# Kernel tuning notes

Measured on AMD Instinct MI355X. Metric: run time of the kernel, lower is better.

## Reference

```python
import jax, jax.numpy as jnp
import numpy as np

I_CH, O_CH = 64, 64
N_NODES, N_EDGES = 20000, 120000


def build_indices(edge_index):
    """Host-side (numpy) replication of the data-dependent index pipeline:
    sort-by-src -> triplets via searchsorted/repeat_interleave -> sort-by-src ->
    prune low-degree half of nodes -> group-by-src (for scatter-mean) -> reindex.
    All shapes depend only on the (constant) int edge_index.
    """
    ei = np.asarray(edge_index)
    ei = ei[:, np.argsort(ei[0], kind='stable')]
    src, tgt = ei[0], ei[1]
    order = np.argsort(tgt, kind='stable')
    stg = tgt[order]
    lb = np.searchsorted(stg, src, side='left')
    ub = np.searchsorted(stg, src, side='right')
    counts = ub - lb
    T = int(counts.sum())
    rep = np.repeat(np.arange(src.shape[0]), counts)
    start = np.cumsum(counts) - counts
    off = np.arange(T) - start[rep]
    hit = order[lb[rep] + off]
    # triplet rows: (SRC[ALL], TGT[ALL], TGT[R])
    tri = np.stack([src[hit], tgt[hit], tgt[rep]])  # [3, T]
    tri = tri[:, np.argsort(tri[0], kind='stable')]
    # remove(): drop edges touching the lowest-degree half of nodes
    deg = np.bincount(tri.ravel())
    low = np.argsort(deg, kind='stable')[: deg.shape[0] // 2]
    keep = np.ones(deg.shape[0], dtype=bool)
    keep[low] = False
    mask = keep[tri[0]] & keep[tri[1]] & keep[tri[2]]
    pos = np.nonzero(mask)[0]
    tri_kept = tri[:, pos]
    # sum(): group kept triplet-edges by source node
    uniq, inv = np.unique(tri_kept[0], return_inverse=True)
    cnt = np.bincount(inv).astype(np.float32)
    # reindex edge_index to compact node ids
    _, new = np.unique(tri_kept, return_inverse=True)
    new_ei = new.reshape(tri_kept.shape).astype(np.int32)
    return tri.astype(np.int32), pos.astype(np.int32), inv.astype(np.int32), int(uniq.shape[0]), cnt, new_ei


def setup_inputs() -> dict:
    key = jax.random.key(0)
    k1, k2, k3, k4 = jax.random.split(key, 4)
    x = jax.random.normal(k1, (N_NODES, I_CH), dtype=jnp.float32)
    edge_index = jax.random.randint(k2, (2, N_EDGES), 0, N_NODES, dtype=jnp.int32)
    # Conv2d(I, O, (3,1)) parameters
    W = 0.05 * jax.random.normal(k3, (O_CH, I_CH, 3, 1), dtype=jnp.float32)
    b = 0.05 * jax.random.normal(k4, (O_CH,), dtype=jnp.float32)
    return {"x": x, "edge_index": edge_index, "W": W, "b": b}


def reference(x, edge_index, W, b):
    tri, pos, inv, U, cnt, new_ei = build_indices(edge_index)
    tri_j = jnp.asarray(tri)
    # gather: INPUT[i,k,t] = x[tri[k,t], i]  -> g is [3, T, I]
    g = x[tri_j]
    # Conv2d(I,O,(3,1)) on [I,3,T] -> [O,1,T]; squeeze the H dim:
    C = jnp.einsum('oik,kti->ot', W[..., 0], g) + b[:, None]  # [O, T]
    Ck = C[:, jnp.asarray(pos)]  # prune edges touching low-degree nodes
    # scatter-mean over destination group (source node of triplet)
    S = jax.ops.segment_sum(Ck.T, jnp.asarray(inv), num_segments=U)  # [U, O]
    x_new = S / jnp.asarray(cnt)[:, None]
    return x_new, jnp.asarray(new_ei)
```

## Files before the change

kernel.cpp:

```cpp
#include <hip/hip_runtime.h>
#include <stdint.h>

typedef uint32_t u32;
typedef unsigned long long u64;

#define LB_TILE 2048

#define S_MAXT 1
#define S_DSTAR 2
#define S_NEED 3
#define S_U 5

__global__ void scan_lb(const u32* __restrict__ in, u32* __restrict__ out, int n,
                        u64* __restrict__ desc){
  __shared__ u32 sh[256];
  __shared__ u32 shPrefix;
  int tid=threadIdx.x, t=blockIdx.x;
  int base = t*LB_TILE + tid*8;
  u32 v[8]; u32 s=0;
#pragma unroll
  for(int k=0;k<8;k++){ u32 xv=(base+k<n)?in[base+k]:0u; v[k]=s; s+=xv; }
  sh[tid]=s; __syncthreads();
  for(int o=1;o<256;o<<=1){
    u32 y=(tid>=o)?sh[tid-o]:0u;
    __syncthreads();
    sh[tid]+=y;
    __syncthreads();
  }
  u32 tileEx = (tid==0)?0u:sh[tid-1];
  u32 agg = sh[255];
  if(tid==0){
    u32 prefix=0u;
    if(t==0){
      atomicExch(&desc[0], ((u64)agg<<32)|2ull);
    } else {
      atomicExch(&desc[t], ((u64)agg<<32)|1ull);
      int j=t-1;
      while(true){
        u64 d=atomicAdd(&desc[j],0ull);
        u32 st=(u32)d;
        if(st==0u) continue;
        prefix += (u32)(d>>32);
        if(st==2u) break;
        --j;
      }
      atomicExch(&desc[t], ((u64)(prefix+agg)<<32)|2ull);
    }
    shPrefix=prefix;
  }
  __syncthreads();
  u32 p=shPrefix+tileEx;
#pragma unroll
  for(int k=0;k<8;k++){ if(base+k<n) out[base+k]=p+v[k]; }
}

__global__ void rx_hist64(const u64* __restrict__ keys, u32* __restrict__ hist,
                          int B, int shift, int chunk, int hostN,
                          const u32* __restrict__ dCount, int cap){
  __shared__ u32 h[256];
  int n = (hostN>=0) ? hostN : (int)(*dCount<(u32)cap?*dCount:(u32)cap);
  h[threadIdx.x]=0u; __syncthreads();
  int base = blockIdx.x*chunk;
  for(int k=threadIdx.x;k<chunk;k+=256){
    int p = base+k;
    if(p<n){ u32 d=(u32)(keys[p]>>shift)&255u; atomicAdd(&h[d],1u); }
  }
  __syncthreads();
  hist[threadIdx.x*B + blockIdx.x] = h[threadIdx.x];
}

__global__ void rx_scatter64(const u64* __restrict__ keys, u64* __restrict__ okeys,
                             const u32* __restrict__ basep, int B, int shift, int chunk,
                             int hostN, const u32* __restrict__ dCount, int cap){
  __shared__ u32 cnt[256];
  int n = (hostN>=0) ? hostN : (int)(*dCount<(u32)cap?*dCount:(u32)cap);
  int lane = threadIdx.x;
  for(int i=lane;i<256;i+=64) cnt[i]=0u;
  __syncthreads();
  int start = blockIdx.x*chunk;
  int rounds = chunk>>6;
  for(int it=0; it<rounds; ++it){
    int p = start + it*64 + lane;
    bool act = (p<n);
    u64 key = act ? keys[p] : 0ull;
    u32 dig = (u32)(key>>shift)&255u;
    u64 m = __ballot(act ? 1 : 0);
    for(int bb=0;bb<8;bb++){
      u64 bl = __ballot((int)((dig>>bb)&1u));
      m &= ((dig>>bb)&1u) ? bl : ~bl;
    }
    u64 lt = (1ull<<lane) - 1ull;
    u32 rb = (u32)__popcll(m & lt);
    u32 c = cnt[dig];
    if(act && rb==0u) atomicAdd(&cnt[dig], (u32)__popcll(m));
    __syncthreads();
    if(act) okeys[basep[dig*B + blockIdx.x] + c + rb] = key;
  }
}

__global__ void k_hist2(const u32* __restrict__ src, const u32* __restrict__ tgt,
                        u32* cntS, u32* cntT, int E){
  int j=blockIdx.x*256+threadIdx.x;
  if(j<E){ atomicAdd(&cntS[src[j]],1u); atomicAdd(&cntT[tgt[j]],1u); }
}

__global__ void k_deg2(const u32* __restrict__ src, const u32* __restrict__ tgt,
                       const u32* __restrict__ cntS, const u32* __restrict__ cntT,
                       u32* deg, int E){
  int e=blockIdx.x*256+threadIdx.x;
  if(e>=E) return;
  u32 s=src[e], t=tgt[e];
  u32 w0=cntS[t]; if(w0) atomicAdd(&deg[s], w0);
  u32 w2=cntT[s]; if(w2) atomicAdd(&deg[t], w2);
}

__global__ void k_degNode(const u32* __restrict__ cntS, const u32* __restrict__ cntT,
                          u32* deg, int NN, int* scal){
  int v=blockIdx.x*256+threadIdx.x;
  if(v>=NN) return;
  u32 d = deg[v] + cntS[v]*cntT[v];
  deg[v]=d;
  if(d) atomicMax(&scal[S_MAXT], v);
}

__global__ void k_degHist(const u32* __restrict__ deg, u32* dh, int NN, const int* __restrict__ scal){
  int v=blockIdx.x*256+threadIdx.x;
  if(v>=NN || v>scal[S_MAXT]) return;
  u32 d=deg[v]; if(d>65535u)d=65535u;
  atomicAdd(&dh[d],1u);
}

__global__ void k_find_dstar(const u32* __restrict__ dh, const u32* __restrict__ dhs, int* scal){
  int d=blockIdx.x*256+threadIdx.x;
  if(d>=65536) return;
  long long kk=(((long long)scal[S_MAXT])+1)>>1;
  if(kk==0){ if(d==0){ scal[S_DSTAR]=-1; scal[S_NEED]=0; } return; }
  long long cum=(long long)dhs[d], h=(long long)dh[d];
  if(cum<=kk-1 && kk-1<cum+h){ scal[S_DSTAR]=d; scal[S_NEED]=(int)(kk-cum); }
}

__global__ void k_ef(const u32* __restrict__ deg, u32* ef, int NN, const int* __restrict__ scal){
  int v=blockIdx.x*256+threadIdx.x;
  if(v>NN) return;
  ef[v] = (v<NN && v<=scal[S_MAXT] && (int)deg[v]==scal[S_DSTAR]) ? 1u:0u;
}

__global__ void k_keep(const u32* __restrict__ deg, const u32* __restrict__ rankEq,
                       u32* keep, int NN, const int* __restrict__ scal){
  int v=blockIdx.x*256+threadIdx.x;
  if(v>=NN) return;
  int d=(int)deg[v]; int ds=scal[S_DSTAR]; int need=scal[S_NEED];
  u32 kp=1u;
  if(d<ds) kp=0u;
  else if(d==ds && (int)rankEq[v]<need) kp=0u;
  keep[v]=kp;
}

__global__ void k_keptCnt(const u32* __restrict__ src, const u32* __restrict__ tgt,
                          const u32* __restrict__ keep, u32* kc, int E){
  int j=blockIdx.x*256+threadIdx.x;
  if(j<E && keep[src[j]]) atomicAdd(&kc[tgt[j]],1u);
}

__global__ void k_mk_ek(const u32* __restrict__ src, const u32* __restrict__ tgt,
                        u64* ek, int E){
  int j=blockIdx.x*256+threadIdx.x;
  if(j<E) ek[j]=((u64)src[j]<<20)|(u64)tgt[j];
}

__global__ void k_mk_a2(const u64* __restrict__ eks, u64* a2, int E){
  int j=blockIdx.x*256+threadIdx.x;
  if(j<E) a2[j]=((eks[j]&0xFFFFFull)<<20)|(u64)j;
}

__global__ void k_cntk(const u64* __restrict__ eks, const u32* __restrict__ keep,
                       const u32* __restrict__ keptCnt, u32* cntk, int E){
  int e=blockIdx.x*256+threadIdx.x;
  if(e>E) return;
  if(e==E){ cntk[e]=0u; return; }
  u64 ke=eks[e];
  u32 s=(u32)(ke>>20), te=(u32)(ke&0xFFFFFull);
  cntk[e] = (keep[s]&keep[te]) ? keptCnt[s] : 0u;
}

__global__ void k_gen_trik(const u64* __restrict__ eks, const u64* __restrict__ a2s,
                           const u32* __restrict__ rp_tgt, const u32* __restrict__ keep,
                           const u32* __restrict__ startk, u64* __restrict__ trig,
                           int E, int cap){
  int e=blockIdx.x*256+threadIdx.x;
  if(e>=E) return;
  u32 c0=startk[e], c1=startk[e+1];
  if(c0>=c1) return;
  u64 ke=eks[e];
  u32 s=(u32)(ke>>20), te=(u32)(ke&0xFFFFFull);
  u32 lb=rp_tgt[s], ub=rp_tgt[s+1];
  u32 idx=c0;
  for(u32 i=lb; i<ub && idx<c1; ++i){
    u32 h=(u32)(a2s[i]&0xFFFFFull);
    u32 hs=(u32)(eks[h]>>20);
    if(keep[hs]){
      if(idx<(u32)cap) trig[idx]=((u64)hs<<30)|((u64)s<<15)|(u64)te;
      ++idx;
    }
  }
}

__global__ void k_heads_present(const u64* __restrict__ tri, u32* hf, u32* present,
                                const u32* __restrict__ dCount, int cap){
  int Tk=(int)(*dCount<(u32)cap?*dCount:(u32)cap);
  int q=blockIdx.x*256+threadIdx.x;
  if(q>cap) return;
  u32 f=0u;
  if(q<Tk){
    u64 key=tri[q];
    f = (q==0 || (key>>30)!=(tri[q-1]>>30)) ? 1u:0u;
    present[key>>30]=1u; present[(key>>15)&0x7FFFu]=1u; present[key&0x7FFFu]=1u;
  }
  hf[q]=f;
}

__global__ void k_gs2(const u32* __restrict__ hf, const u32* __restrict__ hs,
                      u32* gs, int* scal, const u32* __restrict__ dCount, int cap){
  int Tk=(int)(*dCount<(u32)cap?*dCount:(u32)cap);
  int q=blockIdx.x*256+threadIdx.x;
  if(q==0){ int U=(int)hs[Tk]; scal[S_U]=U; gs[U]=(u32)Tk; }
  if(q>=Tk) return;
  if(hf[q]) gs[hs[q+1]-1u]=(u32)q;
}

__global__ void k_write_ei(const u64* __restrict__ tri, const u32* __restrict__ newid,
                           float* out, const int* __restrict__ scal,
                           const u32* __restrict__ dCount, int cap, int out_size){
  int Tk=(int)(*dCount<(u32)cap?*dCount:(u32)cap);
  int q=blockIdx.x*256+threadIdx.x;
  if(q>=Tk) return;
  u64 key=tri[q];
  int bs=scal[S_U]*64;
  int i0=bs+q, i1=bs+Tk+q, i2=bs+2*Tk+q;
  if(i0<out_size) out[i0]=(float)newid[key>>30];
  if(i1<out_size) out[i1]=(float)newid[(key>>15)&0x7FFFu];
  if(i2<out_size) out[i2]=(float)newid[key&0x7FFFu];
}

__global__ __launch_bounds__(256) void k_xnew3(const float* __restrict__ x,
    const float* __restrict__ W, const float* __restrict__ b,
    const u64* __restrict__ tri, const u32* __restrict__ gs,
    float* __restrict__ out, const int* __restrict__ scal){
  __shared__ float Wl[192*65];
  __shared__ float sv[4][192];
  int tid=threadIdx.x;
  for(int j=tid;j<12288;j+=256){
    int r=j%192, o=j/192;
    Wl[r*65+o]=W[j];
  }
  __syncthreads();
  int U=scal[S_U];
  int w=tid>>6, lane=tid&63;
  float bv=b[lane];
  for(int g=blockIdx.x*4+w; g<U; g+=gridDim.x*4){
    u32 q0=gs[g], q1=gs[g+1];
    float a1=0.f,a2=0.f;
    for(u32 q=q0;q<q1;q++){
      u64 key=tri[q];
      a1 += x[(size_t)((key>>15)&0x7FFFull)*64+lane];
      a2 += x[(size_t)(key&0x7FFFull)*64+lane];
    }
    float xu = x[(size_t)(tri[q0]>>30)*64+lane];
    sv[w][lane]=xu; sv[w][64+lane]=a1; sv[w][128+lane]=a2;
    float acc0=0.f, acc12=0.f;
#pragma unroll 4
    for(int ii=0;ii<64;ii++){
      acc0  += Wl[(ii*3+0)*65+lane]*sv[w][ii];
      acc12 += Wl[(ii*3+1)*65+lane]*sv[w][64+ii]
             + Wl[(ii*3+2)*65+lane]*sv[w][128+ii];
    }
    out[(size_t)g*64+lane] = bv + acc0 + acc12/(float)(q1-q0);
  }
}

extern "C" void kernel_launch(void* const* d_in, const int* in_sizes, int n_in,
                              void* d_out, int out_size, void* d_ws, size_t ws_size,
                              hipStream_t stream){
  const float* x = (const float*)d_in[0];
  const int*   ei = (const int*)d_in[1];
  const float* W = (const float*)d_in[2];
  const float* b = (const float*)d_in[3];
  int NN = in_sizes[0]/64;
  int E  = in_sizes[1]/2;
  const u32* src=(const u32*)ei;
  const u32* tgt=(const u32*)(ei+E);

  int KCAP = ((out_size/3 + 1023)/1024)*1024; if(KCAP<1024) KCAP=1024;

  char* base=(char*)d_ws; size_t off=0;
  auto alloc=[&](size_t nInts)->u32*{
    u32* p=(u32*)(base+off);
    off += ( (nInts*4 + 255) & ~(size_t)255 );
    return p;
  };
  int* scal=(int*)alloc(64);
  u32* cntT=alloc(NN+1); u32* cntS=alloc(NN);
  u32* deg=alloc(NN); u32* degHist=alloc(65536);
  u32* present=alloc(NN+1); u32* keptCnt=alloc(NN);
  u64* desc=(u64*)alloc(8192);
  size_t zoneBytes = off;
  u64* ekA=(u64*)alloc(2*(size_t)E); u64* ekB=(u64*)alloc(2*(size_t)E);
  u64* a2A=(u64*)alloc(2*(size_t)E);
  u64* triA=(u64*)alloc(2*(size_t)KCAP); u64* triB=(u64*)alloc(2*(size_t)KCAP);
  u32* rp_tgt=alloc(NN+1);
  u32* cntk=alloc(E+1); u32* startk=alloc(E+1);
  u32* degHistScan=alloc(65536);
  u32* ef=alloc(NN+1); u32* rankEq=alloc(NN+1); u32* keep=alloc(NN);
  u32* newid=alloc(NN+1); u32* gs=alloc(NN+2);
  u32* hf=alloc(KCAP+1); u32* hs=alloc(KCAP+1);
  u32* rxhist=alloc(65536);
  if(off > ws_size) return;
  u64* a2B=ekB;

  size_t descUsed=0;
  auto scan_ex=[&](const u32* in, u32* out, int n){
    int nb=(n+LB_TILE-1)/LB_TILE;
    scan_lb<<<nb,256,0,stream>>>(in,out,n,desc+descUsed);
    descUsed += (size_t)nb;
  };
  auto rx_pass2=[&](const u64* kin, u64* kout, int B, int shift, int chunk,
                    int hostN, const u32* dCount, int cap){
    rx_hist64<<<B,256,0,stream>>>(kin,rxhist,B,shift,chunk,hostN,dCount,cap);
    scan_ex(rxhist,rxhist,256*B);
    rx_scatter64<<<B,64,0,stream>>>(kin,kout,rxhist,B,shift,chunk,hostN,dCount,cap);
  };

  int gE=(E+255)/256, gE1=(E+256)/256;
  int gNN=(NN+255)/256, gNN1=(NN+256)/256;
  int gKC=(KCAP+255)/256, gKC1=(KCAP+256)/256;
  int BE=(E+511)/512;
  int B3=KCAP/1024;

  hipMemsetAsync(base,0,zoneBytes,stream);

  k_hist2<<<gE,256,0,stream>>>(src,tgt,cntS,cntT,E);
  k_deg2<<<gE,256,0,stream>>>(src,tgt,cntS,cntT,deg,E);
  k_degNode<<<gNN,256,0,stream>>>(cntS,cntT,deg,NN,scal);
  k_degHist<<<gNN,256,0,stream>>>(deg,degHist,NN,scal);
  scan_ex(degHist,degHistScan,65536);
  k_find_dstar<<<256,256,0,stream>>>(degHist,degHistScan,scal);
  k_ef<<<gNN1,256,0,stream>>>(deg,ef,NN,scal);
  scan_ex(ef,rankEq,NN+1);
  k_keep<<<gNN,256,0,stream>>>(deg,rankEq,keep,NN,scal);
  k_keptCnt<<<gE,256,0,stream>>>(src,tgt,keep,keptCnt,E);

  scan_ex(cntT,rp_tgt,NN+1);

  k_mk_ek<<<gE,256,0,stream>>>(src,tgt,ekA,E);
  rx_pass2(ekA,ekB,BE,20,512,E,nullptr,0);
  rx_pass2(ekB,ekA,BE,28,512,E,nullptr,0);

  k_mk_a2<<<gE,256,0,stream>>>(ekA,a2A,E);
  rx_pass2(a2A,a2B,BE,20,512,E,nullptr,0);
  rx_pass2(a2B,a2A,BE,28,512,E,nullptr,0);

  k_cntk<<<gE1,256,0,stream>>>(ekA,keep,keptCnt,cntk,E);
  scan_ex(cntk,startk,E+1);

  k_gen_trik<<<gE,256,0,stream>>>(ekA,a2A,rp_tgt,keep,startk,triA,E,KCAP);

  rx_pass2(triA,triB,B3,30,1024,-1,startk+E,KCAP);
  rx_pass2(triB,triA,B3,38,1024,-1,startk+E,KCAP);

  k_heads_present<<<gKC1,256,0,stream>>>(triA,hf,present,startk+E,KCAP);
  scan_ex(hf,hs,KCAP+1);
  scan_ex(present,newid,NN+1);
  k_gs2<<<gKC,256,0,stream>>>(hf,hs,gs,scal,startk+E,KCAP);

  float* outF=(float*)d_out;
  k_write_ei<<<gKC,256,0,stream>>>(triA,newid,outF,scal,startk+E,KCAP,out_size);
  k_xnew3<<<768,256,0,stream>>>(x,W,b,triA,gs,outF,scal);
}
```

Before: 375.5 us.

## Replace radix sorts with onesweep passes and split gather-sum from matmul

Replaces the hist/scan/scatter radix sort triple with a single-kernel onesweep pass that uses decoupled lookback per digit, with the global digit histograms precomputed. Two separate edge sorts are merged into one 4-pass sort over a combined (tgt,src,idx) key. Several small degree and dstar kernels are fused, and the newid and head scans are combined into one scan. The per-group neighbour sum is moved into a load-balanced atomic kernel ahead of the matvec. The aim is fewer launches and better balance across groups, at the cost of extra float atomics, a large zeroed workspace, and spin-wait lookback.

```diff
diff --git a/kernel.cpp b/kernel.cpp
--- a/kernel.cpp
+++ b/kernel.cpp
@@ -5,6 +5,8 @@
 typedef unsigned long long u64;
 
 #define LB_TILE 2048
+#define OW_TILE 1024
+#define RUN 32
 
 #define S_MAXT 1
 #define S_DSTAR 2
@@ -54,89 +56,182 @@
   for(int k=0;k<8;k++){ if(base+k<n) out[base+k]=p+v[k]; }
 }
 
-__global__ void rx_hist64(const u64* __restrict__ keys, u32* __restrict__ hist,
-                          int B, int shift, int chunk, int hostN,
-                          const u32* __restrict__ dCount, int cap){
-  __shared__ u32 h[256];
-  int n = (hostN>=0) ? hostN : (int)(*dCount<(u32)cap?*dCount:(u32)cap);
-  h[threadIdx.x]=0u; __syncthreads();
-  int base = blockIdx.x*chunk;
-  for(int k=threadIdx.x;k<chunk;k+=256){
-    int p = base+k;
-    if(p<n){ u32 d=(u32)(keys[p]>>shift)&255u; atomicAdd(&h[d],1u); }
-  }
-  __syncthreads();
-  hist[threadIdx.x*B + blockIdx.x] = h[threadIdx.x];
-}
-
-__global__ void rx_scatter64(const u64* __restrict__ keys, u64* __restrict__ okeys,
-                             const u32* __restrict__ basep, int B, int shift, int chunk,
-                             int hostN, const u32* __restrict__ dCount, int cap){
-  __shared__ u32 cnt[256];
-  int n = (hostN>=0) ? hostN : (int)(*dCount<(u32)cap?*dCount:(u32)cap);
-  int lane = threadIdx.x;
-  for(int i=lane;i<256;i+=64) cnt[i]=0u;
-  __syncthreads();
-  int start = blockIdx.x*chunk;
-  int rounds = chunk>>6;
-  for(int it=0; it<rounds; ++it){
-    int p = start + it*64 + lane;
-    bool act = (p<n);
-    u64 key = act ? keys[p] : 0ull;
-    u32 dig = (u32)(key>>shift)&255u;
-    u64 m = __ballot(act ? 1 : 0);
+__global__ __launch_bounds__(256) void ow_pass(const u64* __restrict__ in,
+    u64* __restrict__ outk, const u32* __restrict__ gbase, u64* __restrict__ desc,
+    int shift, int hostN, const u32* __restrict__ dCount, int cap){
+  __shared__ u32 hist[256], bd[256], cnt2[256];
+  __shared__ u32 cnt4[4][256];
+  int n = (hostN>=0)?hostN:(int)((*dCount)<(u32)cap?(*dCount):(u32)cap);
+  int tid=threadIdx.x, b=blockIdx.x, w=tid>>6, lane=tid&63;
+  int base=b*OW_TILE;
+  hist[tid]=0u; cnt2[tid]=0u;
+  cnt4[0][tid]=0u; cnt4[1][tid]=0u; cnt4[2][tid]=0u; cnt4[3][tid]=0u;
+  __syncthreads();
+  u64 k[4]; bool act[4];
+#pragma unroll
+  for(int i=0;i<4;i++){
+    int p=base+i*256+tid; act[i]=(p<n);
+    k[i]=act[i]?in[p]:0ull;
+    if(act[i]) atomicAdd(&hist[(u32)(k[i]>>shift)&255u],1u);
+  }
+  __syncthreads();
+  u32 agg=hist[tid];
+  if(b==0){
+    atomicExch(&desc[tid], ((u64)agg<<32)|2ull);
+    bd[tid]=gbase[tid];
+  } else {
+    atomicExch(&desc[(size_t)b*256+tid], ((u64)agg<<32)|1ull);
+    u32 pre=0u; int j=b-1;
+    while(true){
+      u64 d=atomicAdd(&desc[(size_t)j*256+tid],0ull);
+      u32 st=(u32)d;
+      if(st==0u) continue;
+      pre+=(u32)(d>>32);
+      if(st==2u) break;
+      --j;
+    }
+    atomicExch(&desc[(size_t)b*256+tid], ((u64)(pre+agg)<<32)|2ull);
+    bd[tid]=gbase[tid]+pre;
+  }
+  __syncthreads();
+#pragma unroll
+  for(int i=0;i<4;i++){
+    u32 dig=(u32)(k[i]>>shift)&255u;
+    u64 m=__ballot(act[i]?1:0);
     for(int bb=0;bb<8;bb++){
-      u64 bl = __ballot((int)((dig>>bb)&1u));
-      m &= ((dig>>bb)&1u) ? bl : ~bl;
-    }
-    u64 lt = (1ull<<lane) - 1ull;
-    u32 rb = (u32)__popcll(m & lt);
-    u32 c = cnt[dig];
-    if(act && rb==0u) atomicAdd(&cnt[dig], (u32)__popcll(m));
-    __syncthreads();
-    if(act) okeys[basep[dig*B + blockIdx.x] + c + rb] = key;
-  }
-}
-
-__global__ void k_hist2(const u32* __restrict__ src, const u32* __restrict__ tgt,
-                        u32* cntS, u32* cntT, int E){
+      u64 bl=__ballot((int)((dig>>bb)&1u));
+      m &= ((dig>>bb)&1u)?bl:~bl;
+    }
+    u32 rb=(u32)__popcll(m&((1ull<<lane)-1ull));
+    if(act[i]&&rb==0u) cnt4[w][dig]=(u32)__popcll(m);
+    __syncthreads();
+    if(act[i]){
+      u32 off=cnt2[dig]+rb;
+      for(int w2=0;w2<w;w2++) off+=cnt4[w2][dig];
+      outk[bd[dig]+off]=k[i];
+    }
+    __syncthreads();
+    cnt2[tid]+=cnt4[0][tid]+cnt4[1][tid]+cnt4[2][tid]+cnt4[3][tid];
+    cnt4[0][tid]=0u; cnt4[1][tid]=0u; cnt4[2][tid]=0u; cnt4[3][tid]=0u;
+    __syncthreads();
+  }
+}
+
+__global__ void k_prehistE(const u64* __restrict__ keys, u32* __restrict__ hg, int n){
+  __shared__ u32 h[4][256];
+  int tid=threadIdx.x;
+  for(int i=0;i<4;i++) h[i][tid]=0u;
+  __syncthreads();
+#pragma unroll
+  for(int i=0;i<4;i++){
+    int p=blockIdx.x*OW_TILE+i*256+tid;
+    if(p<n){
+      u64 key=keys[p];
+      atomicAdd(&h[0][(u32)(key>>24)&255u],1u);
+      atomicAdd(&h[1][(u32)(key>>32)&255u],1u);
+      atomicAdd(&h[2][(u32)(key>>40)&255u],1u);
+      atomicAdd(&h[3][(u32)(key>>48)&255u],1u);
+    }
+  }
+  __syncthreads();
+  for(int i=0;i<4;i++) if(h[i][tid]) atomicAdd(&hg[i*256+tid],h[i][tid]);
+}
+
+__global__ void k_prehistT(const u64* __restrict__ keys, u32* __restrict__ hg,
+                           const u32* __restrict__ dCount, int cap){
+  __shared__ u32 h[2][256];
+  int n=(int)((*dCount)<(u32)cap?(*dCount):(u32)cap);
+  int tid=threadIdx.x;
+  h[0][tid]=0u; h[1][tid]=0u;
+  __syncthreads();
+#pragma unroll
+  for(int i=0;i<4;i++){
+    int p=blockIdx.x*OW_TILE+i*256+tid;
+    if(p<n){
+      u64 key=keys[p];
+      atomicAdd(&h[0][(u32)(key>>30)&255u],1u);
+      atomicAdd(&h[1][(u32)(key>>38)&255u],1u);
+    }
+  }
+  __syncthreads();
+  if(h[0][tid]) atomicAdd(&hg[tid],h[0][tid]);
+  if(h[1][tid]) atomicAdd(&hg[256+tid],h[1][tid]);
+}
+
+__global__ void k_scan256(const u32* __restrict__ hg, u32* __restrict__ gb, int H){
+  __shared__ u32 sh[256];
+  int t=threadIdx.x;
+  for(int hh=0;hh<H;hh++){
+    u32 v=hg[hh*256+t];
+    sh[t]=v; __syncthreads();
+    for(int o=1;o<256;o<<=1){
+      u32 y=(t>=o)?sh[t-o]:0u; __syncthreads();
+      sh[t]+=y; __syncthreads();
+    }
+    gb[hh*256+t]=sh[t]-v;
+    __syncthreads();
+  }
+}
+
+__global__ void k_edge0(const u32* __restrict__ src, const u32* __restrict__ tgt,
+                        u32* cntS, u32* cntT, u64* keyA, int E){
   int j=blockIdx.x*256+threadIdx.x;
-  if(j<E){ atomicAdd(&cntS[src[j]],1u); atomicAdd(&cntT[tgt[j]],1u); }
-}
-
-__global__ void k_deg2(const u32* __restrict__ src, const u32* __restrict__ tgt,
-                       const u32* __restrict__ cntS, const u32* __restrict__ cntT,
-                       u32* deg, int E){
+  if(j>=E) return;
+  u32 s=src[j], t=tgt[j];
+  atomicAdd(&cntS[s],1u); atomicAdd(&cntT[t],1u);
+  keyA[j]=((u64)t<<40)|((u64)s<<24)|(u64)j;
+}
+
+__global__ void k_deg2m(const u32* __restrict__ src, const u32* __restrict__ tgt,
+                        const u32* __restrict__ cntS, const u32* __restrict__ cntT,
+                        u32* deg, int* scal, int E){
+  __shared__ int mx;
+  if(threadIdx.x==0) mx=-1;
+  __syncthreads();
   int e=blockIdx.x*256+threadIdx.x;
-  if(e>=E) return;
-  u32 s=src[e], t=tgt[e];
-  u32 w0=cntS[t]; if(w0) atomicAdd(&deg[s], w0);
-  u32 w2=cntT[s]; if(w2) atomicAdd(&deg[t], w2);
-}
-
-__global__ void k_degNode(const u32* __restrict__ cntS, const u32* __restrict__ cntT,
-                          u32* deg, int NN, int* scal){
+  int loc=-1;
+  if(e<E){
+    u32 s=src[e], t=tgt[e];
+    u32 w0=cntS[t], w2=cntT[s];
+    if(w0){ atomicAdd(&deg[s],w0); loc=(int)(s>t?s:t); }
+    if(w2){ atomicAdd(&deg[t],w2); if((int)t>loc) loc=(int)t; }
+  }
+  if(loc>=0) atomicMax(&mx,loc);
+  __syncthreads();
+  if(threadIdx.x==0 && mx>=0) atomicMax(&scal[S_MAXT],mx);
+}
+
+__global__ void k_degNodeHist(const u32* __restrict__ cntS, const u32* __restrict__ cntT,
+                              u32* deg, u32* dh, int NN, const int* __restrict__ scal){
   int v=blockIdx.x*256+threadIdx.x;
   if(v>=NN) return;
-  u32 d = deg[v] + cntS[v]*cntT[v];
+  u32 d=deg[v]+cntS[v]*cntT[v];
   deg[v]=d;
-  if(d) atomicMax(&scal[S_MAXT], v);
-}
-
-__global__ void k_degHist(const u32* __restrict__ deg, u32* dh, int NN, const int* __restrict__ scal){
-  int v=blockIdx.x*256+threadIdx.x;
-  if(v>=NN || v>scal[S_MAXT]) return;
-  u32 d=deg[v]; if(d>65535u)d=65535u;
-  atomicAdd(&dh[d],1u);
-}
-
-__global__ void k_find_dstar(const u32* __restrict__ dh, const u32* __restrict__ dhs, int* scal){
-  int d=blockIdx.x*256+threadIdx.x;
-  if(d>=65536) return;
+  if(v<=scal[S_MAXT]){ if(d>65535u)d=65535u; atomicAdd(&dh[d],1u); }
+}
+
+__global__ void k_dstar1b(const u32* __restrict__ dh, int* scal){
+  __shared__ u32 part[256];
+  __shared__ u32 sc[256];
+  int t=threadIdx.x;
   long long kk=(((long long)scal[S_MAXT])+1)>>1;
-  if(kk==0){ if(d==0){ scal[S_DSTAR]=-1; scal[S_NEED]=0; } return; }
-  long long cum=(long long)dhs[d], h=(long long)dh[d];
-  if(cum<=kk-1 && kk-1<cum+h){ scal[S_DSTAR]=d; scal[S_NEED]=(int)(kk-cum); }
+  u32 s=0;
+  for(int i=0;i<256;i++) s+=dh[t*256+i];
+  part[t]=s; sc[t]=s; __syncthreads();
+  for(int o=1;o<256;o<<=1){
+    u32 y=(t>=o)?sc[t-o]:0u; __syncthreads();
+    sc[t]+=y; __syncthreads();
+  }
+  if(kk==0){ if(t==0){ scal[S_DSTAR]=-1; scal[S_NEED]=0; } return; }
+  long long cum=(long long)(sc[t]-part[t]);
+  if(kk-1>=cum && kk-1<cum+(long long)part[t]){
+    long long c=cum;
+    for(int i=0;i<256;i++){
+      u32 h=dh[t*256+i];
+      if(kk-1>=c && kk-1<c+(long long)h){ scal[S_DSTAR]=t*256+i; scal[S_NEED]=(int)(kk-c); break; }
+      c+=h;
+    }
+  }
 }
 
 __global__ void k_ef(const u32* __restrict__ deg, u32* ef, int NN, const int* __restrict__ scal){
@@ -162,89 +257,100 @@
   if(j<E && keep[src[j]]) atomicAdd(&kc[tgt[j]],1u);
 }
 
-__global__ void k_mk_ek(const u32* __restrict__ src, const u32* __restrict__ tgt,
-                        u64* ek, int E){
-  int j=blockIdx.x*256+threadIdx.x;
-  if(j<E) ek[j]=((u64)src[j]<<20)|(u64)tgt[j];
-}
-
-__global__ void k_mk_a2(const u64* __restrict__ eks, u64* a2, int E){
-  int j=blockIdx.x*256+threadIdx.x;
-  if(j<E) a2[j]=((eks[j]&0xFFFFFull)<<20)|(u64)j;
-}
-
-__global__ void k_cntk(const u64* __restrict__ eks, const u32* __restrict__ keep,
+__global__ void k_cntk(const u64* __restrict__ C, const u32* __restrict__ keep,
                        const u32* __restrict__ keptCnt, u32* cntk, int E){
   int e=blockIdx.x*256+threadIdx.x;
   if(e>E) return;
   if(e==E){ cntk[e]=0u; return; }
-  u64 ke=eks[e];
-  u32 s=(u32)(ke>>20), te=(u32)(ke&0xFFFFFull);
-  cntk[e] = (keep[s]&keep[te]) ? keptCnt[s] : 0u;
-}
-
-__global__ void k_gen_trik(const u64* __restrict__ eks, const u64* __restrict__ a2s,
-                           const u32* __restrict__ rp_tgt, const u32* __restrict__ keep,
-                           const u32* __restrict__ startk, u64* __restrict__ trig,
-                           int E, int cap){
+  u64 ke=C[e];
+  u32 s=(u32)(ke>>24)&0xFFFFu, te=(u32)(ke>>40);
+  cntk[e]=(keep[s]&keep[te])?keptCnt[s]:0u;
+}
+
+__global__ void k_gen_trik(const u64* __restrict__ C, const u64* __restrict__ H,
+    const u32* __restrict__ rp_tgt, const u32* __restrict__ keep,
+    const u32* __restrict__ startk, u64* __restrict__ trig, int E, int cap){
   int e=blockIdx.x*256+threadIdx.x;
   if(e>=E) return;
   u32 c0=startk[e], c1=startk[e+1];
   if(c0>=c1) return;
-  u64 ke=eks[e];
-  u32 s=(u32)(ke>>20), te=(u32)(ke&0xFFFFFull);
+  u64 ke=C[e];
+  u32 s=(u32)(ke>>24)&0xFFFFu, te=(u32)(ke>>40);
   u32 lb=rp_tgt[s], ub=rp_tgt[s+1];
   u32 idx=c0;
-  for(u32 i=lb; i<ub && idx<c1; ++i){
-    u32 h=(u32)(a2s[i]&0xFFFFFull);
-    u32 hs=(u32)(eks[h]>>20);
-    if(keep[hs]){
-      if(idx<(u32)cap) trig[idx]=((u64)hs<<30)|((u64)s<<15)|(u64)te;
+  for(u32 i=lb;i<ub&&idx<c1;++i){
+    u64 hk=H[i];
+    u32 hsv=(u32)(hk>>24)&0xFFFFu;
+    if(keep[hsv]){
+      if(idx<(u32)cap) trig[idx]=((u64)hsv<<30)|((u64)s<<15)|(u64)te;
       ++idx;
     }
   }
 }
 
-__global__ void k_heads_present(const u64* __restrict__ tri, u32* hf, u32* present,
-                                const u32* __restrict__ dCount, int cap){
-  int Tk=(int)(*dCount<(u32)cap?*dCount:(u32)cap);
+__global__ void k_heads_present(const u64* __restrict__ tri, u32* __restrict__ hf,
+    u32* __restrict__ present, const u32* __restrict__ dCount, int KC){
+  int Tk=(int)((*dCount)<(u32)KC?(*dCount):(u32)KC);
   int q=blockIdx.x*256+threadIdx.x;
-  if(q>cap) return;
+  if(q>KC) return;
   u32 f=0u;
   if(q<Tk){
     u64 key=tri[q];
-    f = (q==0 || (key>>30)!=(tri[q-1]>>30)) ? 1u:0u;
-    present[key>>30]=1u; present[(key>>15)&0x7FFFu]=1u; present[key&0x7FFFu]=1u;
+    f=(q==0||(key>>30)!=(tri[q-1]>>30))?1u:0u;
+    present[key>>30]=1u;
+    present[(key>>15)&0x7FFFu]=1u;
+    present[key&0x7FFFu]=1u;
   }
   hf[q]=f;
 }
 
-__global__ void k_gs2(const u32* __restrict__ hf, const u32* __restrict__ hs,
-                      u32* gs, int* scal, const u32* __restrict__ dCount, int cap){
-  int Tk=(int)(*dCount<(u32)cap?*dCount:(u32)cap);
+__global__ void k_gs_ei(const u64* __restrict__ tri, const u32* __restrict__ hf,
+    const u32* __restrict__ hsAll, u32* __restrict__ gs, float* __restrict__ out,
+    int* scal, const u32* __restrict__ dCount, int KC, int out_size){
+  int Tk=(int)((*dCount)<(u32)KC?(*dCount):(u32)KC);
+  u32 U=hsAll[KC+1];
   int q=blockIdx.x*256+threadIdx.x;
-  if(q==0){ int U=(int)hs[Tk]; scal[S_U]=U; gs[U]=(u32)Tk; }
+  if(q==0){ scal[S_U]=(int)U; gs[U]=(u32)Tk; }
   if(q>=Tk) return;
-  if(hf[q]) gs[hs[q+1]-1u]=(u32)q;
-}
-
-__global__ void k_write_ei(const u64* __restrict__ tri, const u32* __restrict__ newid,
-                           float* out, const int* __restrict__ scal,
-                           const u32* __restrict__ dCount, int cap, int out_size){
-  int Tk=(int)(*dCount<(u32)cap?*dCount:(u32)cap);
-  int q=blockIdx.x*256+threadIdx.x;
-  if(q>=Tk) return;
+  if(hf[q]) gs[hsAll[q+1]-1u]=(u32)q;
   u64 key=tri[q];
-  int bs=scal[S_U]*64;
+  int bs=(int)U*64;
   int i0=bs+q, i1=bs+Tk+q, i2=bs+2*Tk+q;
-  if(i0<out_size) out[i0]=(float)newid[key>>30];
-  if(i1<out_size) out[i1]=(float)newid[(key>>15)&0x7FFFu];
-  if(i2<out_size) out[i2]=(float)newid[key&0x7FFFu];
-}
-
-__global__ __launch_bounds__(256) void k_xnew3(const float* __restrict__ x,
+  if(i0<out_size) out[i0]=(float)(hsAll[(size_t)KC+1+(size_t)(key>>30)]-U);
+  if(i1<out_size) out[i1]=(float)(hsAll[(size_t)KC+1+(size_t)((key>>15)&0x7FFFu)]-U);
+  if(i2<out_size) out[i2]=(float)(hsAll[(size_t)KC+1+(size_t)(key&0x7FFFu)]-U);
+}
+
+__global__ __launch_bounds__(256) void k_xsum(const float* __restrict__ x,
+    const u64* __restrict__ tri, const u32* __restrict__ hs,
+    float* __restrict__ S1, float* __restrict__ S2,
+    const u32* __restrict__ dCount, int KC){
+  int Tk=(int)((*dCount)<(u32)KC?(*dCount):(u32)KC);
+  int w=threadIdx.x>>6, lane=threadIdx.x&63;
+  int r=blockIdx.x*4+w;
+  int q0=r*RUN; if(q0>=Tk) return;
+  int q1=q0+RUN; if(q1>Tk)q1=Tk;
+  int gcur=(int)hs[q0+1]-1;
+  float a1=0.f,a2=0.f;
+  for(int q=q0;q<q1;q++){
+    int g=(int)hs[q+1]-1;
+    if(g!=gcur){
+      atomicAdd(&S1[(size_t)gcur*64+lane],a1);
+      atomicAdd(&S2[(size_t)gcur*64+lane],a2);
+      a1=0.f;a2=0.f;gcur=g;
+    }
+    u64 key=tri[q];
+    a1+=x[(size_t)((key>>15)&0x7FFFull)*64+lane];
+    a2+=x[(size_t)(key&0x7FFFull)*64+lane];
+  }
+  atomicAdd(&S1[(size_t)gcur*64+lane],a1);
+  atomicAdd(&S2[(size_t)gcur*64+lane],a2);
+}
+
+__global__ __launch_bounds__(256) void k_xmat(const float* __restrict__ x,
     const float* __restrict__ W, const float* __restrict__ b,
     const u64* __restrict__ tri, const u32* __restrict__ gs,
+    const float* __restrict__ S1, const float* __restrict__ S2,
     float* __restrict__ out, const int* __restrict__ scal){
   __shared__ float Wl[192*65];
   __shared__ float sv[4][192];
@@ -259,14 +365,10 @@
   float bv=b[lane];
   for(int g=blockIdx.x*4+w; g<U; g+=gridDim.x*4){
     u32 q0=gs[g], q1=gs[g+1];
-    float a1=0.f,a2=0.f;
-    for(u32 q=q0;q<q1;q++){
-      u64 key=tri[q];
-      a1 += x[(size_t)((key>>15)&0x7FFFull)*64+lane];
-      a2 += x[(size_t)(key&0x7FFFull)*64+lane];
-    }
-    float xu = x[(size_t)(tri[q0]>>30)*64+lane];
-    sv[w][lane]=xu; sv[w][64+lane]=a1; sv[w][128+lane]=a2;
+    u32 uniq=(u32)(tri[q0]>>30);
+    sv[w][lane]=x[(size_t)uniq*64+lane];
+    sv[w][64+lane]=S1[(size_t)g*64+lane];
+    sv[w][128+lane]=S2[(size_t)g*64+lane];
     float acc0=0.f, acc12=0.f;
 #pragma unroll 4
     for(int ii=0;ii<64;ii++){
@@ -290,7 +392,9 @@
   const u32* src=(const u32*)ei;
   const u32* tgt=(const u32*)(ei+E);
 
-  int KCAP = ((out_size/3 + 1023)/1024)*1024; if(KCAP<1024) KCAP=1024;
+  int KC = ((out_size/3 + OW_TILE-1)/OW_TILE)*OW_TILE; if(KC<OW_TILE) KC=OW_TILE;
+  int B_E=(E+OW_TILE-1)/OW_TILE;
+  int B_T=KC/OW_TILE;
 
   char* base=(char*)d_ws; size_t off=0;
   auto alloc=[&](size_t nInts)->u32*{
@@ -301,78 +405,74 @@
   int* scal=(int*)alloc(64);
   u32* cntT=alloc(NN+1); u32* cntS=alloc(NN);
   u32* deg=alloc(NN); u32* degHist=alloc(65536);
-  u32* present=alloc(NN+1); u32* keptCnt=alloc(NN);
-  u64* desc=(u64*)alloc(8192);
+  u32* keptCnt=alloc(NN);
+  u32* histGE=alloc(4*256); u32* histGT=alloc(2*256);
+  u64* descS=(u64*)alloc(2*1024);
+  u64* descE=(u64*)alloc(2*(size_t)(4*B_E*256));
+  u64* descT=(u64*)alloc(2*(size_t)(2*B_T*256));
+  u32* hfp=alloc((size_t)KC+1+NN+1);
+  float* S1=(float*)alloc((size_t)NN*64);
+  float* S2=(float*)alloc((size_t)NN*64);
   size_t zoneBytes = off;
-  u64* ekA=(u64*)alloc(2*(size_t)E); u64* ekB=(u64*)alloc(2*(size_t)E);
-  u64* a2A=(u64*)alloc(2*(size_t)E);
-  u64* triA=(u64*)alloc(2*(size_t)KCAP); u64* triB=(u64*)alloc(2*(size_t)KCAP);
+  u64* bufA=(u64*)alloc(2*(size_t)E);
+  u64* bufB=(u64*)alloc(2*(size_t)E);
+  u64* bufC=(u64*)alloc(2*(size_t)E);
+  u64* triA=(u64*)alloc(2*(size_t)KC); u64* triB=(u64*)alloc(2*(size_t)KC);
   u32* rp_tgt=alloc(NN+1);
   u32* cntk=alloc(E+1); u32* startk=alloc(E+1);
-  u32* degHistScan=alloc(65536);
+  u32* gbaseE=alloc(4*256); u32* gbaseT=alloc(2*256);
   u32* ef=alloc(NN+1); u32* rankEq=alloc(NN+1); u32* keep=alloc(NN);
-  u32* newid=alloc(NN+1); u32* gs=alloc(NN+2);
-  u32* hf=alloc(KCAP+1); u32* hs=alloc(KCAP+1);
-  u32* rxhist=alloc(65536);
+  u32* gs=alloc(NN+2);
+  u32* hsAll=alloc((size_t)KC+1+NN+1);
   if(off > ws_size) return;
-  u64* a2B=ekB;
+
+  u32* hf=hfp; u32* present=hfp+(KC+1);
+  const u32* dCount=startk+E;
 
   size_t descUsed=0;
   auto scan_ex=[&](const u32* in, u32* out, int n){
     int nb=(n+LB_TILE-1)/LB_TILE;
-    scan_lb<<<nb,256,0,stream>>>(in,out,n,desc+descUsed);
+    scan_lb<<<nb,256,0,stream>>>(in,out,n,descS+descUsed);
     descUsed += (size_t)nb;
   };
-  auto rx_pass2=[&](const u64* kin, u64* kout, int B, int shift, int chunk,
-                    int hostN, const u32* dCount, int cap){
-    rx_hist64<<<B,256,0,stream>>>(kin,rxhist,B,shift,chunk,hostN,dCount,cap);
-    scan_ex(rxhist,rxhist,256*B);
-    rx_scatter64<<<B,64,0,stream>>>(kin,kout,rxhist,B,shift,chunk,hostN,dCount,cap);
-  };
 
   int gE=(E+255)/256, gE1=(E+256)/256;
   int gNN=(NN+255)/256, gNN1=(NN+256)/256;
-  int gKC=(KCAP+255)/256, gKC1=(KCAP+256)/256;
-  int BE=(E+511)/512;
-  int B3=KCAP/1024;
+  int gKC=(KC+255)/256, gKC1=(KC+256)/256;
 
   hipMemsetAsync(base,0,zoneBytes,stream);
 
-  k_hist2<<<gE,256,0,stream>>>(src,tgt,cntS,cntT,E);
-  k_deg2<<<gE,256,0,stream>>>(src,tgt,cntS,cntT,deg,E);
-  k_degNode<<<gNN,256,0,stream>>>(cntS,cntT,deg,NN,scal);
-  k_degHist<<<gNN,256,0,stream>>>(deg,degHist,NN,scal);
-  scan_ex(degHist,degHistScan,65536);
-  k_find_dstar<<<256,256,0,stream>>>(degHist,degHistScan,scal);
+  k_edge0<<<gE,256,0,stream>>>(src,tgt,cntS,cntT,bufA,E);
+  k_deg2m<<<gE,256,0,stream>>>(src,tgt,cntS,cntT,deg,scal,E);
+  k_degNodeHist<<<gNN,256,0,stream>>>(cntS,cntT,deg,degHist,NN,scal);
+  k_dstar1b<<<1,256,0,stream>>>(degHist,scal);
   k_ef<<<gNN1,256,0,stream>>>(deg,ef,NN,scal);
   scan_ex(ef,rankEq,NN+1);
   k_keep<<<gNN,256,0,stream>>>(deg,rankEq,keep,NN,scal);
   k_keptCnt<<<gE,256,0,stream>>>(src,tgt,keep,keptCnt,E);
-
   scan_ex(cntT,rp_tgt,NN+1);
 
-  k_mk_ek<<<gE,256,0,stream>>>(src,tgt,ekA,E);
-  rx_pass2(ekA,ekB,BE,20,512,E,nullptr,0);
-  rx_pass2(ekB,ekA,BE,28,512,E,nullptr,0);
-
-  k_mk_a2<<<gE,256,0,stream>>>(ekA,a2A,E);
-  rx_pass2(a2A,a2B,BE,20,512,E,nullptr,0);
-  rx_pass2(a2B,a2A,BE,28,512,E,nullptr,0);
-
-  k_cntk<<<gE1,256,0,stream>>>(ekA,keep,keptCnt,cntk,E);
+  k_prehistE<<<B_E,256,0,stream>>>(bufA,histGE,E);
+  k_scan256<<<1,256,0,stream>>>(histGE,gbaseE,4);
+  ow_pass<<<B_E,256,0,stream>>>(bufA,bufB,gbaseE+0*256,descE+(size_t)0*B_E*256,24,E,nullptr,0);
+  ow_pass<<<B_E,256,0,stream>>>(bufB,bufC,gbaseE+1*256,descE+(size_t)1*B_E*256,32,E,nullptr,0);
+  ow_pass<<<B_E,256,0,stream>>>(bufC,bufA,gbaseE+2*256,descE+(size_t)2*B_E*256,40,E,nullptr,0);
+  ow_pass<<<B_E,256,0,stream>>>(bufA,bufB,gbaseE+3*256,descE+(size_t)3*B_E*256,48,E,nullptr,0);
+
+  k_cntk<<<gE1,256,0,stream>>>(bufC,keep,keptCnt,cntk,E);
   scan_ex(cntk,startk,E+1);
-
-  k_gen_trik<<<gE,256,0,stream>>>(ekA,a2A,rp_tgt,keep,startk,triA,E,KCAP);
-
-  rx_pass2(triA,triB,B3,30,1024,-1,startk+E,KCAP);
-  rx_pass2(triB,triA,B3,38,1024,-1,startk+E,KCAP);
-
-  k_heads_present<<<gKC1,256,0,stream>>>(triA,hf,present,startk+E,KCAP);
-  scan_ex(hf,hs,KCAP+1);
-  scan_ex(present,newid,NN+1);
-  k_gs2<<<gKC,256,0,stream>>>(hf,hs,gs,scal,startk+E,KCAP);
-
+  k_gen_trik<<<gE,256,0,stream>>>(bufC,bufB,rp_tgt,keep,startk,triA,E,KC);
+
+  k_prehistT<<<B_T,256,0,stream>>>(triA,histGT,dCount,KC);
+  k_scan256<<<1,256,0,stream>>>(histGT,gbaseT,2);
+  ow_pass<<<B_T,256,0,stream>>>(triA,triB,gbaseT+0*256,descT+(size_t)0*B_T*256,30,-1,dCount,KC);
+  ow_pass<<<B_T,256,0,stream>>>(triB,triA,gbaseT+1*256,descT+(size_t)1*B_T*256,38,-1,dCount,KC);
+
+  k_heads_present<<<gKC1,256,0,stream>>>(triA,hf,present,dCount,KC);
+  scan_ex(hfp,hsAll,KC+1+NN+1);
   float* outF=(float*)d_out;
-  k_write_ei<<<gKC,256,0,stream>>>(triA,newid,outF,scal,startk+E,KCAP,out_size);
-  k_xnew3<<<768,256,0,stream>>>(x,W,b,triA,gs,outF,scal);
-}
+  k_gs_ei<<<gKC,256,0,stream>>>(triA,hf,hsAll,gs,outF,scal,dCount,KC,out_size);
+
+  k_xsum<<<KC/(4*RUN),256,0,stream>>>(x,triA,hsAll,S1,S2,dCount,KC);
+  k_xmat<<<768,256,0,stream>>>(x,W,b,triA,gs,S1,S2,outF,scal);
+}
```

Measured after the change: 337.3 us. 10.2% less time.
